# Kernel optimization log

Measured on AMD Instinct MI355X. Metric: run time of the kernel, lower is better.

## Reference

```python
import jax, jax.numpy as jnp
import numpy as np
import math

B, S, D, H, W = 1, 2048, 512, 8, 64
DK = D // H
NEG = -1e9


def setup_inputs() -> dict:
    rng = jax.random.key(0)
    ks = jax.random.split(rng, 8)
    sc = 0.02
    return {
        "query": jax.random.normal(ks[0], (B, S, D), jnp.float32),
        "key": jax.random.normal(ks[1], (B, S, D), jnp.float32),
        "value": jax.random.normal(ks[2], (B, S, D), jnp.float32),
        "Wq": jax.random.normal(ks[3], (D, D), jnp.float32) * sc,
        "Wk": jax.random.normal(ks[4], (D, D), jnp.float32) * sc,
        "Wv": jax.random.normal(ks[5], (D, D), jnp.float32) * sc,
        "Wo": jax.random.normal(ks[6], (D, D), jnp.float32) * sc,
        "bo": jax.random.normal(ks[7], (D,), jnp.float32) * sc,
    }


def reference(query, key, value, Wq, Wk, Wv, Wo, bo):
    b, s, d = query.shape

    def proj(x, Wm):
        # [B,S,D] -> [B,H,S,DK]
        return (x @ Wm.T).reshape(b, s, H, DK).transpose(0, 2, 1, 3)

    Q = proj(query, Wq)
    K = proj(key, Wk)
    V = proj(value, Wv)

    i = jnp.arange(s)
    rel = jnp.arange(-W, 1)                     # causal band: keys i-W..i
    idx = i[:, None] + rel[None, :]             # [S, W+1]
    valid = idx >= 0
    idxc = jnp.clip(idx, 0, s - 1)

    Kw = K[:, :, idxc, :]                       # [B,H,S,W+1,DK]
    Vw = V[:, :, idxc, :]

    scores = jnp.einsum('bhsd,bhsrd->bhsr', Q, Kw) / math.sqrt(DK)
    decay_bias = 0.1 * jnp.exp(-0.1 * jnp.abs(rel.astype(jnp.float32)))
    scores = jnp.where(valid[None, None], scores + decay_bias, NEG)
    probs = jax.nn.softmax(scores, axis=-1)     # [B,H,S,W+1]

    out = jnp.einsum('bhsr,bhsrd->bhsd', probs, Vw)
    out = out.transpose(0, 2, 1, 3).reshape(b, s, d)
    output = out @ Wo.T + bo

    # attention_weights [B,H,S,2W]: only rows with window_size <= 2W are written
    win = jnp.minimum(s, i + W + 1) - jnp.maximum(0, i - W)   # [S]
    stored = win <= 2 * W
    slot = jnp.arange(2 * W)
    ridx = slot[None, :] + jnp.maximum(W - i, 0)[:, None]     # [S,2W] slot->band index
    vmask = (ridx <= W) & (slot[None, :] < win[:, None]) & stored[:, None]
    gath = jnp.take_along_axis(probs, jnp.clip(ridx, 0, W)[None, None], axis=-1)
    attn_w = jnp.where(vmask[None, None], gath, 0.0)

    return output, attn_w
```

## Files before the change

kernel.cpp:

```cpp
#include <hip/hip_runtime.h>
#include <stdint.h>

#define SEQ   2048
#define DM    512
#define NHEAD 8
#define DKH   64
#define WIN   64
#define NEGV  -1000000000.0f

typedef __attribute__((ext_vector_type(8))) short          short8;
typedef __attribute__((ext_vector_type(4))) float          float4v;
typedef __attribute__((ext_vector_type(8))) unsigned short ushort8v;

__device__ __forceinline__ unsigned short f2bf(float x) {
    uint32_t u = __float_as_uint(x);
    uint32_t r = (u + 0x7FFFu + ((u >> 16) & 1u)) >> 16;
    return (unsigned short)r;
}
__device__ __forceinline__ float bf2f(unsigned short u) {
    return __uint_as_float(((uint32_t)u) << 16);
}

template<bool A_F32, bool B_F32, bool BIAS, bool OUT_BF16, int BM, int BN>
__device__ __forceinline__ void gemm_body(const void* __restrict__ Ap,
                                          const void* __restrict__ Bp,
                                          const float* __restrict__ bias,
                                          void* __restrict__ Cv)
{
    __shared__ __align__(16) unsigned short As[2][BM * 32];
    __shared__ __align__(16) unsigned short Bs[2][BN * 32];

    constexpr int HA = (BM * 32) / (256 * 8);
    constexpr int HB = (BN * 32) / (256 * 8);
    constexpr int FM = BM / 32;
    constexpr int FN = BN / 32;

    const int tid  = threadIdx.x;
    const int m0   = blockIdx.x * BM;
    const int n0   = blockIdx.y * BN;
    const int lane = tid & 63;
    const int wave = tid >> 6;
    const int wm   = (wave >> 1) * (BM / 2);
    const int wn   = (wave & 1) * (BN / 2);
    const int lm   = lane & 15;
    const int lk   = (lane >> 4) * 8;

    float4v acc[FM][FN] = {};

    float4   raf[HA][2]; ushort8v rab[HA];
    float4   rbf[HB][2]; ushort8v rbb[HB];

    auto load_regs = [&](int k0) {
        #pragma unroll
        for (int h = 0; h < HA; h++) {
            int c = tid + h * 256;
            int r = c >> 2, kc = (c & 3) * 8;
            if constexpr (A_F32) {
                const float* p = (const float*)Ap + (size_t)(m0 + r) * 512 + k0 + kc;
                raf[h][0] = *(const float4*)p;
                raf[h][1] = *(const float4*)(p + 4);
            } else {
                rab[h] = *(const ushort8v*)((const unsigned short*)Ap +
                                            (size_t)(m0 + r) * 512 + k0 + kc);
            }
        }
        #pragma unroll
        for (int h = 0; h < HB; h++) {
            int c = tid + h * 256;
            int r = c >> 2, kc = (c & 3) * 8;
            if constexpr (B_F32) {
                const float* p = (const float*)Bp + (size_t)(n0 + r) * 512 + k0 + kc;
                rbf[h][0] = *(const float4*)p;
                rbf[h][1] = *(const float4*)(p + 4);
            } else {
                rbb[h] = *(const ushort8v*)((const unsigned short*)Bp +
                                            (size_t)(n0 + r) * 512 + k0 + kc);
            }
        }
    };
    auto store_lds = [&](int buf) {
        #pragma unroll
        for (int h = 0; h < HA; h++) {
            int c = tid + h * 256;
            int r = c >> 2, kc = (c & 3) * 8;
            ushort8v o;
            if constexpr (A_F32) {
                o[0] = f2bf(raf[h][0].x); o[1] = f2bf(raf[h][0].y);
                o[2] = f2bf(raf[h][0].z); o[3] = f2bf(raf[h][0].w);
                o[4] = f2bf(raf[h][1].x); o[5] = f2bf(raf[h][1].y);
                o[6] = f2bf(raf[h][1].z); o[7] = f2bf(raf[h][1].w);
            } else {
                o = rab[h];
            }
            *(ushort8v*)&As[buf][r * 32 + kc] = o;
        }
        #pragma unroll
        for (int h = 0; h < HB; h++) {
            int c = tid + h * 256;
            int r = c >> 2, kc = (c & 3) * 8;
            ushort8v o;
            if constexpr (B_F32) {
                o[0] = f2bf(rbf[h][0].x); o[1] = f2bf(rbf[h][0].y);
                o[2] = f2bf(rbf[h][0].z); o[3] = f2bf(rbf[h][0].w);
                o[4] = f2bf(rbf[h][1].x); o[5] = f2bf(rbf[h][1].y);
                o[6] = f2bf(rbf[h][1].z); o[7] = f2bf(rbf[h][1].w);
            } else {
                o = rbb[h];
            }
            *(ushort8v*)&Bs[buf][r * 32 + kc] = o;
        }
    };

    load_regs(0);
    store_lds(0);
    load_regs(32);
    __syncthreads();

    for (int t = 0; t < 16; ++t) {
        const int cur = t & 1;
        short8 av[FM], bv[FN];
        #pragma unroll
        for (int mt = 0; mt < FM; mt++)
            av[mt] = *(const short8*)&As[cur][(wm + mt * 16 + lm) * 32 + lk];
        #pragma unroll
        for (int nt = 0; nt < FN; nt++)
            bv[nt] = *(const short8*)&Bs[cur][(wn + nt * 16 + lm) * 32 + lk];
        #pragma unroll
        for (int mt = 0; mt < FM; mt++)
            #pragma unroll
            for (int nt = 0; nt < FN; nt++)
                acc[mt][nt] = __builtin_amdgcn_mfma_f32_16x16x32_bf16(
                    av[mt], bv[nt], acc[mt][nt], 0, 0, 0);
        if (t < 15) {
            store_lds(cur ^ 1);
            if (t < 14) load_regs((t + 2) * 32);
        }
        __syncthreads();
    }

    const int r0 = (lane >> 4) * 4;
    const int cn = lane & 15;
    #pragma unroll
    for (int nt = 0; nt < FN; nt++) {
        int gcol = n0 + wn + nt * 16 + cn;
        float b = BIAS ? bias[gcol] : 0.f;
        #pragma unroll
        for (int mt = 0; mt < FM; mt++) {
            int grow = m0 + wm + mt * 16 + r0;
            #pragma unroll
            for (int reg = 0; reg < 4; reg++) {
                float val = acc[mt][nt][reg] + b;
                if (OUT_BF16)
                    ((unsigned short*)Cv)[(size_t)(grow + reg) * 512 + gcol] = f2bf(val);
                else
                    ((float*)Cv)[(size_t)(grow + reg) * 512 + gcol] = val;
            }
        }
    }
}

__global__ __launch_bounds__(256)
void qkv_gemm_kernel(const float* __restrict__ q, const float* __restrict__ k,
                     const float* __restrict__ v, const float* __restrict__ wq,
                     const float* __restrict__ wk, const float* __restrict__ wv,
                     unsigned short* __restrict__ Qp, unsigned short* __restrict__ Kp,
                     unsigned short* __restrict__ Vp)
{
    const float *A, *B; unsigned short* C;
    if (blockIdx.z == 0)      { A = q; B = wq; C = Qp; }
    else if (blockIdx.z == 1) { A = k; B = wk; C = Kp; }
    else                      { A = v; B = wv; C = Vp; }
    gemm_body<true, true, false, true, 64, 64>(A, B, nullptr, C);
}

__global__ __launch_bounds__(256)
void out_gemm_kernel(const unsigned short* __restrict__ ctxb,
                     const float* __restrict__ wo,
                     const float* __restrict__ bo, float* __restrict__ out)
{
    gemm_body<false, true, true, false, 64, 64>(ctxb, wo, bo, out);
}

#define VTS 152

__global__ __launch_bounds__(256)
void attn_kernel(const unsigned short* __restrict__ Qp,
                 const unsigned short* __restrict__ Kp,
                 const unsigned short* __restrict__ Vp,
                 unsigned short* __restrict__ ctxb,
                 float* __restrict__ attnw)
{
    __shared__ __align__(16) unsigned short Qs[64 * 72];
    __shared__ __align__(16) unsigned short Ks[128 * 72];
    __shared__ __align__(16) unsigned short Vt[64 * VTS];
    __shared__ __align__(16) unsigned short Ps[4][16][96];

    const int h   = blockIdx.y;
    const int q0  = blockIdx.x * 64;
    const int tid = threadIdx.x;

    for (int c = tid; c < 512; c += 256) {
        int row = c >> 3, ch = c & 7;
        *(ushort8v*)&Qs[row * 72 + ch * 8] =
            *(const ushort8v*)&Qp[(size_t)(q0 + row) * 512 + h * 64 + ch * 8];
    }
    for (int c = tid; c < 1024; c += 256) {
        int row = c >> 3, ch = c & 7;
        int g = q0 - 64 + row;
        ushort8v val = {0, 0, 0, 0, 0, 0, 0, 0};
        if (g >= 0)
            val = *(const ushort8v*)&Kp[(size_t)g * 512 + h * 64 + ch * 8];
        *(ushort8v*)&Ks[row * 72 + ch * 8] = val;
    }
    {
        int key = tid >> 1, dh = tid & 1;
        int g = q0 - 64 + key;
        ushort8v vv[4];
        #pragma unroll
        for (int j = 0; j < 4; j++) {
            ushort8v z = {0, 0, 0, 0, 0, 0, 0, 0};
            vv[j] = (g >= 0)
                ? *(const ushort8v*)&Vp[(size_t)g * 512 + h * 64 + dh * 32 + j * 8]
                : z;
        }
        #pragma unroll
        for (int j = 0; j < 4; j++)
            #pragma unroll
            for (int e = 0; e < 8; e++)
                Vt[(dh * 32 + j * 8 + e) * VTS + key] = vv[j][e];
    }
    for (int t = tid; t < 64 * 24; t += 256) {
        int d = t / 24, c = 128 + (t % 24);
        Vt[d * VTS + c] = 0;
    }
    __syncthreads();

    const int lane = tid & 63;
    const int w    = tid >> 6;
    const int lm   = lane & 15;
    const int g16  = lane >> 4;
    const int lk8  = g16 * 8;

    short8 av0 = *(const short8*)&Qs[(w * 16 + lm) * 72 + lk8];
    short8 av1 = *(const short8*)&Qs[(w * 16 + lm) * 72 + 32 + lk8];
    float4v sc[5];
    #pragma unroll
    for (int kt = 0; kt < 5; kt++) {
        const unsigned short* kr = &Ks[(w * 16 + kt * 16 + lm) * 72];
        short8 b0 = *(const short8*)(kr + lk8);
        short8 b1 = *(const short8*)(kr + 32 + lk8);
        float4v a = {0.f, 0.f, 0.f, 0.f};
        a = __builtin_amdgcn_mfma_f32_16x16x32_bf16(av0, b0, a, 0, 0, 0);
        a = __builtin_amdgcn_mfma_f32_16x16x32_bf16(av1, b1, a, 0, 0, 0);
        sc[kt] = a;
    }

    float v[5][4];
    #pragma unroll
    for (int kt = 0; kt < 5; kt++) {
        int kk = kt * 16 + lm;
        int g  = q0 - 64 + w * 16 + kk;
        #pragma unroll
        for (int reg = 0; reg < 4; reg++) {
            int rr = g16 * 4 + reg;
            bool valid = (kk >= rr) && (kk <= rr + 64) && (g >= 0);
            v[kt][reg] = valid
                ? sc[kt][reg] * 0.125f + 0.1f * __expf(-0.1f * (float)(64 + rr - kk))
                : NEGV;
        }
    }

    float mx[4], sm[4];
    #pragma unroll
    for (int reg = 0; reg < 4; reg++) {
        float m = v[0][reg];
        #pragma unroll
        for (int kt = 1; kt < 5; kt++) m = fmaxf(m, v[kt][reg]);
        mx[reg] = m;
    }
    #pragma unroll
    for (int off = 1; off < 16; off <<= 1)
        #pragma unroll
        for (int reg = 0; reg < 4; reg++)
            mx[reg] = fmaxf(mx[reg], __shfl_xor(mx[reg], off));
    float p[5][4];
    #pragma unroll
    for (int reg = 0; reg < 4; reg++) {
        float s = 0.f;
        #pragma unroll
        for (int kt = 0; kt < 5; kt++) {
            float e = __expf(v[kt][reg] - mx[reg]);
            p[kt][reg] = e;
            s += e;
        }
        sm[reg] = s;
    }
    #pragma unroll
    for (int off = 1; off < 16; off <<= 1)
        #pragma unroll
        for (int reg = 0; reg < 4; reg++)
            sm[reg] += __shfl_xor(sm[reg], off);
    #pragma unroll
    for (int reg = 0; reg < 4; reg++) {
        float inv = 1.f / sm[reg];
        #pragma unroll
        for (int kt = 0; kt < 5; kt++) p[kt][reg] *= inv;
    }

    #pragma unroll
    for (int kt = 0; kt < 5; kt++)
        #pragma unroll
        for (int reg = 0; reg < 4; reg++)
            Ps[w][g16 * 4 + reg][kt * 16 + lm] = f2bf(p[kt][reg]);
    #pragma unroll
    for (int reg = 0; reg < 4; reg++)
        Ps[w][g16 * 4 + reg][80 + lm] = 0;

    __syncthreads();

    float4v oacc[4] = {};
    #pragma unroll
    for (int ks = 0; ks < 3; ks++) {
        short8 pa = *(const short8*)&Ps[w][lm][ks * 32 + lk8];
        #pragma unroll
        for (int nt = 0; nt < 4; nt++) {
            short8 vb = *(const short8*)&Vt[(nt * 16 + lm) * VTS + w * 16 + ks * 32 + lk8];
            oacc[nt] = __builtin_amdgcn_mfma_f32_16x16x32_bf16(pa, vb, oacc[nt], 0, 0, 0);
        }
    }

    #pragma unroll
    for (int nt = 0; nt < 4; nt++)
        #pragma unroll
        for (int reg = 0; reg < 4; reg++) {
            int i = q0 + w * 16 + g16 * 4 + reg;
            ctxb[(size_t)i * 512 + h * 64 + nt * 16 + lm] = f2bf(oacc[nt][reg]);
        }

    __syncthreads();

    for (int t = tid; t < 1024; t += 256) {
        int ql = t >> 4;
        int s0 = (t & 15) * 8;
        int i  = q0 + ql;
        float4 v0 = {0.f, 0.f, 0.f, 0.f}, v1 = {0.f, 0.f, 0.f, 0.f};
        if (q0 == 0) {
            #pragma unroll
            for (int e = 0; e < 8; e++) {
                int slot = s0 + e;
                if (slot <= ql) {
                    int kk = (ql & 15) + slot + 64 - ql;
                    float vv = bf2f(Ps[ql >> 4][ql & 15][kk]);
                    if (e < 4) ((float*)&v0)[e] = vv; else ((float*)&v1)[e - 4] = vv;
                }
            }
        } else if (q0 == SEQ - 64) {
            #pragma unroll
            for (int e = 0; e < 8; e++) {
                int slot = s0 + e;
                if (slot <= 64) {
                    int kk = (ql & 15) + slot;
                    float vv = bf2f(Ps[ql >> 4][ql & 15][kk]);
                    if (e < 4) ((float*)&v0)[e] = vv; else ((float*)&v1)[e - 4] = vv;
                }
            }
        }
        float* dst = &attnw[((size_t)h * SEQ + i) * 2 * WIN + s0];
        *(float4*)dst       = v0;
        *(float4*)(dst + 4) = v1;
    }
}

extern "C" void kernel_launch(void* const* d_in, const int* in_sizes, int n_in,
                              void* d_out, int out_size, void* d_ws, size_t ws_size,
                              hipStream_t stream)
{
    const float* query = (const float*)d_in[0];
    const float* key   = (const float*)d_in[1];
    const float* value = (const float*)d_in[2];
    const float* Wq    = (const float*)d_in[3];
    const float* Wk    = (const float*)d_in[4];
    const float* Wv    = (const float*)d_in[5];
    const float* Wo    = (const float*)d_in[6];
    const float* bo    = (const float*)d_in[7];

    float* out   = (float*)d_out;
    float* attnw = out + SEQ * DM;

    unsigned short* Qp   = (unsigned short*)d_ws;
    unsigned short* Kp   = Qp + 1048576;
    unsigned short* Vp   = Kp + 1048576;
    unsigned short* ctxb = Vp + 1048576;

    dim3 g1(SEQ / 64, DM / 64, 3);
    qkv_gemm_kernel<<<g1, 256, 0, stream>>>(query, key, value, Wq, Wk, Wv, Qp, Kp, Vp);

    dim3 g2(SEQ / 64, NHEAD);
    attn_kernel<<<g2, 256, 0, stream>>>(Qp, Kp, Vp, ctxb, attnw);

    dim3 g3(SEQ / 64, DM / 64);
    out_gemm_kernel<<<g3, 256, 0, stream>>>(ctxb, Wo, bo, out);
}
```

Measured before the change: 103.9 us.

## Deepen GEMM K-step to 64 with swizzled LDS, vectorize V transpose, reorder attention tail

The shared GEMM body now stages 64-wide K tiles with an XOR swizzle on the LDS layout. This halves the number of main-loop iterations and barriers and is meant to cut LDS bank conflicts. In the attention kernel, the V transpose into LDS now writes 4-element vectors, the padding is zeroed with 16-byte stores, and the attention-weight store loop is moved before the PV matmul, which removes one barrier. These are several loosely related changes, and the larger LDS tiles raise shared-memory use per block.

```diff
diff --git a/kernel.cpp b/kernel.cpp
--- a/kernel.cpp
+++ b/kernel.cpp
@@ -11,6 +11,7 @@
 typedef __attribute__((ext_vector_type(8))) short          short8;
 typedef __attribute__((ext_vector_type(4))) float          float4v;
 typedef __attribute__((ext_vector_type(8))) unsigned short ushort8v;
+typedef __attribute__((ext_vector_type(4))) unsigned short ushort4v;
 
 __device__ __forceinline__ unsigned short f2bf(float x) {
     uint32_t u = __float_as_uint(x);
@@ -21,119 +22,123 @@
     return __uint_as_float(((uint32_t)u) << 16);
 }
 
-template<bool A_F32, bool B_F32, bool BIAS, bool OUT_BF16, int BM, int BN>
+template<bool A_F32, bool B_F32, bool BIAS, bool OUT_BF16>
 __device__ __forceinline__ void gemm_body(const void* __restrict__ Ap,
                                           const void* __restrict__ Bp,
                                           const float* __restrict__ bias,
                                           void* __restrict__ Cv)
 {
-    __shared__ __align__(16) unsigned short As[2][BM * 32];
-    __shared__ __align__(16) unsigned short Bs[2][BN * 32];
-
-    constexpr int HA = (BM * 32) / (256 * 8);
-    constexpr int HB = (BN * 32) / (256 * 8);
-    constexpr int FM = BM / 32;
-    constexpr int FN = BN / 32;
+    __shared__ __align__(16) unsigned short As[2][64 * 64];
+    __shared__ __align__(16) unsigned short Bs[2][64 * 64];
 
     const int tid  = threadIdx.x;
-    const int m0   = blockIdx.x * BM;
-    const int n0   = blockIdx.y * BN;
+    const int m0   = blockIdx.x * 64;
+    const int n0   = blockIdx.y * 64;
     const int lane = tid & 63;
     const int wave = tid >> 6;
-    const int wm   = (wave >> 1) * (BM / 2);
-    const int wn   = (wave & 1) * (BN / 2);
+    const int wm   = (wave >> 1) * 32;
+    const int wn   = (wave & 1) * 32;
     const int lm   = lane & 15;
-    const int lk   = (lane >> 4) * 8;
-
-    float4v acc[FM][FN] = {};
-
-    float4   raf[HA][2]; ushort8v rab[HA];
-    float4   rbf[HB][2]; ushort8v rbb[HB];
+    const int cg   = lane >> 4;
+
+    float4v acc[2][2] = {};
+
+    float4   raf[2][2]; ushort8v rab[2];
+    float4   rbf[2][2]; ushort8v rbb[2];
 
     auto load_regs = [&](int k0) {
         #pragma unroll
-        for (int h = 0; h < HA; h++) {
-            int c = tid + h * 256;
-            int r = c >> 2, kc = (c & 3) * 8;
+        for (int hh = 0; hh < 2; hh++) {
+            int c = tid + hh * 256;
+            int r = c >> 3, kc = (c & 7) * 8;
             if constexpr (A_F32) {
                 const float* p = (const float*)Ap + (size_t)(m0 + r) * 512 + k0 + kc;
-                raf[h][0] = *(const float4*)p;
-                raf[h][1] = *(const float4*)(p + 4);
+                raf[hh][0] = *(const float4*)p;
+                raf[hh][1] = *(const float4*)(p + 4);
             } else {
-                rab[h] = *(const ushort8v*)((const unsigned short*)Ap +
-                                            (size_t)(m0 + r) * 512 + k0 + kc);
-            }
-        }
-        #pragma unroll
-        for (int h = 0; h < HB; h++) {
-            int c = tid + h * 256;
-            int r = c >> 2, kc = (c & 3) * 8;
+                rab[hh] = *(const ushort8v*)((const unsigned short*)Ap +
+                                             (size_t)(m0 + r) * 512 + k0 + kc);
+            }
+        }
+        #pragma unroll
+        for (int hh = 0; hh < 2; hh++) {
+            int c = tid + hh * 256;
+            int r = c >> 3, kc = (c & 7) * 8;
             if constexpr (B_F32) {
                 const float* p = (const float*)Bp + (size_t)(n0 + r) * 512 + k0 + kc;
-                rbf[h][0] = *(const float4*)p;
-                rbf[h][1] = *(const float4*)(p + 4);
+                rbf[hh][0] = *(const float4*)p;
+                rbf[hh][1] = *(const float4*)(p + 4);
             } else {
-                rbb[h] = *(const ushort8v*)((const unsigned short*)Bp +
-                                            (size_t)(n0 + r) * 512 + k0 + kc);
+                rbb[hh] = *(const ushort8v*)((const unsigned short*)Bp +
+                                             (size_t)(n0 + r) * 512 + k0 + kc);
             }
         }
     };
     auto store_lds = [&](int buf) {
         #pragma unroll
-        for (int h = 0; h < HA; h++) {
-            int c = tid + h * 256;
-            int r = c >> 2, kc = (c & 3) * 8;
+        for (int hh = 0; hh < 2; hh++) {
+            int c = tid + hh * 256;
+            int r = c >> 3, ck = c & 7;
+            int off = r * 64 + ((ck ^ ((r & 1) << 2)) << 3);
             ushort8v o;
             if constexpr (A_F32) {
-                o[0] = f2bf(raf[h][0].x); o[1] = f2bf(raf[h][0].y);
-                o[2] = f2bf(raf[h][0].z); o[3] = f2bf(raf[h][0].w);
-                o[4] = f2bf(raf[h][1].x); o[5] = f2bf(raf[h][1].y);
-                o[6] = f2bf(raf[h][1].z); o[7] = f2bf(raf[h][1].w);
+                o[0] = f2bf(raf[hh][0].x); o[1] = f2bf(raf[hh][0].y);
+                o[2] = f2bf(raf[hh][0].z); o[3] = f2bf(raf[hh][0].w);
+                o[4] = f2bf(raf[hh][1].x); o[5] = f2bf(raf[hh][1].y);
+                o[6] = f2bf(raf[hh][1].z); o[7] = f2bf(raf[hh][1].w);
             } else {
-                o = rab[h];
-            }
-            *(ushort8v*)&As[buf][r * 32 + kc] = o;
-        }
-        #pragma unroll
-        for (int h = 0; h < HB; h++) {
-            int c = tid + h * 256;
-            int r = c >> 2, kc = (c & 3) * 8;
+                o = rab[hh];
+            }
+            *(ushort8v*)&As[buf][off] = o;
+        }
+        #pragma unroll
+        for (int hh = 0; hh < 2; hh++) {
+            int c = tid + hh * 256;
+            int r = c >> 3, ck = c & 7;
+            int off = r * 64 + ((ck ^ ((r & 1) << 2)) << 3);
             ushort8v o;
             if constexpr (B_F32) {
-                o[0] = f2bf(rbf[h][0].x); o[1] = f2bf(rbf[h][0].y);
-                o[2] = f2bf(rbf[h][0].z); o[3] = f2bf(rbf[h][0].w);
-                o[4] = f2bf(rbf[h][1].x); o[5] = f2bf(rbf[h][1].y);
-                o[6] = f2bf(rbf[h][1].z); o[7] = f2bf(rbf[h][1].w);
+                o[0] = f2bf(rbf[hh][0].x); o[1] = f2bf(rbf[hh][0].y);
+                o[2] = f2bf(rbf[hh][0].z); o[3] = f2bf(rbf[hh][0].w);
+                o[4] = f2bf(rbf[hh][1].x); o[5] = f2bf(rbf[hh][1].y);
+                o[6] = f2bf(rbf[hh][1].z); o[7] = f2bf(rbf[hh][1].w);
             } else {
-                o = rbb[h];
-            }
-            *(ushort8v*)&Bs[buf][r * 32 + kc] = o;
+                o = rbb[hh];
+            }
+            *(ushort8v*)&Bs[buf][off] = o;
         }
     };
 
     load_regs(0);
     store_lds(0);
-    load_regs(32);
+    load_regs(64);
     __syncthreads();
 
-    for (int t = 0; t < 16; ++t) {
+    for (int t = 0; t < 8; ++t) {
         const int cur = t & 1;
-        short8 av[FM], bv[FN];
-        #pragma unroll
-        for (int mt = 0; mt < FM; mt++)
-            av[mt] = *(const short8*)&As[cur][(wm + mt * 16 + lm) * 32 + lk];
-        #pragma unroll
-        for (int nt = 0; nt < FN; nt++)
-            bv[nt] = *(const short8*)&Bs[cur][(wn + nt * 16 + lm) * 32 + lk];
-        #pragma unroll
-        for (int mt = 0; mt < FM; mt++)
-            #pragma unroll
-            for (int nt = 0; nt < FN; nt++)
-                acc[mt][nt] = __builtin_amdgcn_mfma_f32_16x16x32_bf16(
-                    av[mt], bv[nt], acc[mt][nt], 0, 0, 0);
-        if (t < 15) {
+        short8 av[2][2], bv[2][2];
+        const int swz = (lm & 1) << 2;
+        #pragma unroll
+        for (int kt = 0; kt < 2; kt++) {
+            const int chunk = ((kt * 4 + cg) ^ swz) << 3;
+            #pragma unroll
+            for (int mt = 0; mt < 2; mt++)
+                av[kt][mt] = *(const short8*)&As[cur][(wm + mt * 16 + lm) * 64 + chunk];
+            #pragma unroll
+            for (int nt = 0; nt < 2; nt++)
+                bv[kt][nt] = *(const short8*)&Bs[cur][(wn + nt * 16 + lm) * 64 + chunk];
+        }
+        #pragma unroll
+        for (int kt = 0; kt < 2; kt++)
+            #pragma unroll
+            for (int mt = 0; mt < 2; mt++)
+                #pragma unroll
+                for (int nt = 0; nt < 2; nt++)
+                    acc[mt][nt] = __builtin_amdgcn_mfma_f32_16x16x32_bf16(
+                        av[kt][mt], bv[kt][nt], acc[mt][nt], 0, 0, 0);
+        if (t < 7) {
             store_lds(cur ^ 1);
-            if (t < 14) load_regs((t + 2) * 32);
+            if (t < 6) load_regs((t + 2) * 64);
         }
         __syncthreads();
     }
@@ -141,11 +146,11 @@
     const int r0 = (lane >> 4) * 4;
     const int cn = lane & 15;
     #pragma unroll
-    for (int nt = 0; nt < FN; nt++) {
+    for (int nt = 0; nt < 2; nt++) {
         int gcol = n0 + wn + nt * 16 + cn;
         float b = BIAS ? bias[gcol] : 0.f;
         #pragma unroll
-        for (int mt = 0; mt < FM; mt++) {
+        for (int mt = 0; mt < 2; mt++) {
             int grow = m0 + wm + mt * 16 + r0;
             #pragma unroll
             for (int reg = 0; reg < 4; reg++) {
@@ -170,7 +175,7 @@
     if (blockIdx.z == 0)      { A = q; B = wq; C = Qp; }
     else if (blockIdx.z == 1) { A = k; B = wk; C = Kp; }
     else                      { A = v; B = wv; C = Vp; }
-    gemm_body<true, true, false, true, 64, 64>(A, B, nullptr, C);
+    gemm_body<true, true, false, true>(A, B, nullptr, C);
 }
 
 __global__ __launch_bounds__(256)
@@ -178,7 +183,7 @@
                      const float* __restrict__ wo,
                      const float* __restrict__ bo, float* __restrict__ out)
 {
-    gemm_body<false, true, true, false, 64, 64>(ctxb, wo, bo, out);
+    gemm_body<false, true, true, false>(ctxb, wo, bo, out);
 }
 
 #define VTS 152
@@ -213,25 +218,26 @@
         *(ushort8v*)&Ks[row * 72 + ch * 8] = val;
     }
     {
-        int key = tid >> 1, dh = tid & 1;
-        int g = q0 - 64 + key;
+        int kg = tid & 31, dg = tid >> 5;
         ushort8v vv[4];
         #pragma unroll
         for (int j = 0; j < 4; j++) {
+            int g = q0 - 64 + 4 * kg + j;
             ushort8v z = {0, 0, 0, 0, 0, 0, 0, 0};
             vv[j] = (g >= 0)
-                ? *(const ushort8v*)&Vp[(size_t)g * 512 + h * 64 + dh * 32 + j * 8]
+                ? *(const ushort8v*)&Vp[(size_t)g * 512 + h * 64 + dg * 8]
                 : z;
         }
         #pragma unroll
-        for (int j = 0; j < 4; j++)
-            #pragma unroll
-            for (int e = 0; e < 8; e++)
-                Vt[(dh * 32 + j * 8 + e) * VTS + key] = vv[j][e];
-    }
-    for (int t = tid; t < 64 * 24; t += 256) {
-        int d = t / 24, c = 128 + (t % 24);
-        Vt[d * VTS + c] = 0;
+        for (int e = 0; e < 8; e++) {
+            ushort4v o = { vv[0][e], vv[1][e], vv[2][e], vv[3][e] };
+            *(ushort4v*)&Vt[(dg * 8 + e) * VTS + 4 * kg] = o;
+        }
+    }
+    if (tid < 192) {
+        int r = tid / 3, c = tid - r * 3;
+        ushort8v z = {0, 0, 0, 0, 0, 0, 0, 0};
+        *(ushort8v*)&Vt[r * VTS + 128 + c * 8] = z;
     }
     __syncthreads();
 
@@ -318,27 +324,6 @@
 
     __syncthreads();
 
-    float4v oacc[4] = {};
-    #pragma unroll
-    for (int ks = 0; ks < 3; ks++) {
-        short8 pa = *(const short8*)&Ps[w][lm][ks * 32 + lk8];
-        #pragma unroll
-        for (int nt = 0; nt < 4; nt++) {
-            short8 vb = *(const short8*)&Vt[(nt * 16 + lm) * VTS + w * 16 + ks * 32 + lk8];
-            oacc[nt] = __builtin_amdgcn_mfma_f32_16x16x32_bf16(pa, vb, oacc[nt], 0, 0, 0);
-        }
-    }
-
-    #pragma unroll
-    for (int nt = 0; nt < 4; nt++)
-        #pragma unroll
-        for (int reg = 0; reg < 4; reg++) {
-            int i = q0 + w * 16 + g16 * 4 + reg;
-            ctxb[(size_t)i * 512 + h * 64 + nt * 16 + lm] = f2bf(oacc[nt][reg]);
-        }
-
-    __syncthreads();
-
     for (int t = tid; t < 1024; t += 256) {
         int ql = t >> 4;
         int s0 = (t & 15) * 8;
@@ -369,6 +354,25 @@
         *(float4*)dst       = v0;
         *(float4*)(dst + 4) = v1;
     }
+
+    float4v oacc[4] = {};
+    #pragma unroll
+    for (int ks = 0; ks < 3; ks++) {
+        short8 pa = *(const short8*)&Ps[w][lm][ks * 32 + lk8];
+        #pragma unroll
+        for (int nt = 0; nt < 4; nt++) {
+            short8 vb = *(const short8*)&Vt[(nt * 16 + lm) * VTS + w * 16 + ks * 32 + lk8];
+            oacc[nt] = __builtin_amdgcn_mfma_f32_16x16x32_bf16(pa, vb, oacc[nt], 0, 0, 0);
+        }
+    }
+
+    #pragma unroll
+    for (int nt = 0; nt < 4; nt++)
+        #pragma unroll
+        for (int reg = 0; reg < 4; reg++) {
+            int i = q0 + w * 16 + g16 * 4 + reg;
+            ctxb[(size_t)i * 512 + h * 64 + nt * 16 + lm] = f2bf(oacc[nt][reg]);
+        }
 }
 
 extern "C" void kernel_launch(void* const* d_in, const int* in_sizes, int n_in,
```

Result: slower. 107.2 us (+3.1%).
